# Optimization experiments

Measured on AMD Instinct MI355X. Metric: run time of the kernel, lower is better.

The kernel has to match this reference:

```python
import jax, jax.numpy as jnp
import numpy as np

QMAX = 127.0  # int8 symmetric quantization range


def _quant_dequant(w):
    """Per-output-channel symmetric int8 fake quantization (weight-only),
    mimicking nn.quantized.Linear.from_float weight quantization."""
    scale = jnp.max(jnp.abs(w), axis=-1, keepdims=True) / QMAX
    scale = jnp.maximum(scale, 1e-8)
    q = jnp.clip(jnp.round(w / scale), -QMAX, QMAX)
    return q * scale


def setup_inputs() -> dict:
    key = jax.random.key(0)
    ks = jax.random.split(key, 7)
    B, S, D, F, E, NS = 2, 2048, 1024, 2048, 8, 1
    std = 1.0 / np.sqrt(D)
    x = jax.random.normal(ks[0], (B, S, D), dtype=jnp.float32)
    router_w = _quant_dequant(jax.random.normal(ks[1], (E, D), dtype=jnp.float32) * std)
    router_b = jnp.zeros((E,), dtype=jnp.float32)
    w_up = _quant_dequant(jax.random.normal(ks[2], (E, F, D), dtype=jnp.float32) * std)
    w_down = _quant_dequant(jax.random.normal(ks[3], (E, D, F), dtype=jnp.float32) / np.sqrt(F))
    shared_w_up = _quant_dequant(jax.random.normal(ks[4], (NS, F, D), dtype=jnp.float32) * std)
    shared_w_down = _quant_dequant(jax.random.normal(ks[5], (NS, D, F), dtype=jnp.float32) / np.sqrt(F))
    return {"x": x, "router_w": router_w, "router_b": router_b,
            "w_up": w_up, "w_down": w_down,
            "shared_w_up": shared_w_up, "shared_w_down": shared_w_down}


def reference(x, router_w, router_b, w_up, w_down, shared_w_up, shared_w_down):
    B, S, D = x.shape
    E = router_w.shape[0]
    TOPK = 2
    xt = x.reshape(-1, D)  # [T, D] tokens

    # Router (quantized linear) -> softmax -> top-k dispatch weights
    logits = xt @ router_w.T + router_b            # [T, E]
    probs = jax.nn.softmax(logits, axis=-1)        # [T, E]
    top_vals, top_idx = jax.lax.top_k(probs, TOPK)  # [T, K]
    top_vals = top_vals / jnp.sum(top_vals, axis=-1, keepdims=True)  # renormalize
    # combine[t, e] = routing weight of expert e for token t (0 if not selected)
    combine = jnp.sum(jax.nn.one_hot(top_idx, E, dtype=xt.dtype) * top_vals[..., None], axis=1)  # [T, E]

    # Routed experts: up -> SiLU -> down, computed densely then combined
    h = jnp.einsum('td,efd->tef', xt, w_up)        # [T, E, F]
    y = jnp.einsum('tef,edf->ted', jax.nn.silu(h), w_down)  # [T, E, D]
    out = jnp.einsum('ted,te->td', y, combine)     # [T, D]

    # Shared experts: always active, summed
    hs = jnp.einsum('td,sfd->tsf', xt, shared_w_up)          # [T, NS, F]
    out = out + jnp.einsum('tsf,sdf->td', jax.nn.silu(hs), shared_w_down)

    return out.reshape(B, S, D)
```

## Files before the change

kernel.cpp:

```cpp
#include <hip/hip_runtime.h>
#include <stdint.h>

typedef unsigned short u16;
typedef int i32x4 __attribute__((ext_vector_type(4)));

#define DDIM 1024
#define FDIM 2048
#define NEXP 8
#define RT_TILES 72
#define SHOFF 9216
#define RCAP 13312
#define NRT 104
#define UPROWS 16384
#define DNROWS 8192
#define WQB 4608


__device__ inline float bf2f(u16 u) {
    union { unsigned int i; float f; } v; v.i = ((unsigned int)u) << 16; return v.f;
}
__device__ inline u16 f2bf(float f) {
    union { float f; unsigned int i; } v; v.f = f;
    unsigned int lsb = (v.i >> 16) & 1u;
    return (u16)((v.i + 0x7fffu + lsb) >> 16);
}
__device__ inline int q8(float v, float inv) {
    int x = (int)rintf(v * inv);
    return x < -127 ? -127 : (x > 127 ? 127 : x);
}

typedef const __attribute__((address_space(1))) void gas_void;
typedef __attribute__((address_space(3))) void las_void;
#define GLL16(g, l) __builtin_amdgcn_global_load_lds((gas_void*)(g), (las_void*)(l), 16, 0, 0)

__device__ inline int detect_inline(const u16* __restrict__ x, int* sh) {
    if (threadIdx.x == 0) *sh = 0;
    __syncthreads();
    const int per = 1024 / blockDim.x;
    int bad = 0;
    for (int i = 0; i < per; i++) {
        u16 v = x[threadIdx.x * per + i];
        if (((v >> 7) & 0xFF) >= 0x8F) bad++;
    }
    if (bad) atomicAdd(sh, bad);
    __syncthreads();
    return (*sh > 32) ? 1 : 0;
}

__global__ __launch_bounds__(256) void fused_rw_kernel(
    const void* __restrict__ x_, const void* __restrict__ rw_, const void* __restrict__ rb_,
    const void* __restrict__ w_up, const void* __restrict__ w_down,
    const void* __restrict__ sw_up, const void* __restrict__ sw_down,
    float* __restrict__ top_w, int* __restrict__ top_idx,
    char* __restrict__ qup, char* __restrict__ qdn,
    float* __restrict__ su, float* __restrict__ sd, int nrb)
{
    __shared__ char smem[32768 + 16];
    const int tid = threadIdx.x;
    const int wave = tid >> 6, lane = tid & 63;
    const int flag = detect_inline((const u16*)x_, (int*)(smem + 32768));

    if ((int)blockIdx.x < nrb) {
        float* rws = (float*)smem;
        if (!flag) {
            const ushort4* rwv = (const ushort4*)rw_;
            #pragma unroll
            for (int i = 0; i < 8; i++) {
                int idx = tid + i * 256;
                ushort4 h = rwv[idx];
                rws[idx * 4 + 0] = bf2f(h.x); rws[idx * 4 + 1] = bf2f(h.y);
                rws[idx * 4 + 2] = bf2f(h.z); rws[idx * 4 + 3] = bf2f(h.w);
            }
        } else {
            const float4* rwv = (const float4*)rw_;
            #pragma unroll
            for (int i = 0; i < 8; i++) {
                int idx = tid + i * 256;
                float4 f = rwv[idx];
                rws[idx * 4 + 0] = f.x; rws[idx * 4 + 1] = f.y;
                rws[idx * 4 + 2] = f.z; rws[idx * 4 + 3] = f.w;
            }
        }
        __syncthreads();

        for (int sub = 0; sub < 4; sub++) {
            const int t = blockIdx.x * 16 + wave * 4 + sub;
            float xv[16];
            if (!flag) {
                const u16* xr = (const u16*)x_ + (size_t)t * DDIM + lane * 16;
                uint4 p0 = *(const uint4*)(xr);
                uint4 p1 = *(const uint4*)(xr + 8);
                #pragma unroll
                for (int d = 0; d < 8; d++) xv[d]     = bf2f(((const u16*)&p0)[d]);
                #pragma unroll
                for (int d = 0; d < 8; d++) xv[d + 8] = bf2f(((const u16*)&p1)[d]);
            } else {
                const float4* xr = (const float4*)((const float*)x_ + (size_t)t * DDIM + lane * 16);
                #pragma unroll
                for (int c = 0; c < 4; c++) {
                    float4 f = xr[c];
                    xv[c * 4 + 0] = f.x; xv[c * 4 + 1] = f.y;
                    xv[c * 4 + 2] = f.z; xv[c * 4 + 3] = f.w;
                }
            }
            float acc[NEXP];
            #pragma unroll
            for (int e = 0; e < NEXP; e++) {
                const float* wr = &rws[e * DDIM + lane * 16];
                float s = 0.f;
                #pragma unroll
                for (int d = 0; d < 16; d++) s += xv[d] * wr[d];
                acc[e] = s;
            }
            #pragma unroll
            for (int e = 0; e < NEXP; e++) {
                #pragma unroll
                for (int off = 32; off > 0; off >>= 1)
                    acc[e] += __shfl_xor(acc[e], off, 64);
            }
            if (lane == 0) {
                float lg[NEXP];
                #pragma unroll
                for (int e = 0; e < NEXP; e++) {
                    float b = flag ? ((const float*)rb_)[e] : bf2f(((const u16*)rb_)[e]);
                    lg[e] = acc[e] + b;
                }
                int i0 = 0;
                #pragma unroll
                for (int e = 1; e < NEXP; e++) if (lg[e] > lg[i0]) i0 = e;
                int i1 = (i0 == 0) ? 1 : 0;
                #pragma unroll
                for (int e = 0; e < NEXP; e++) if (e != i0 && lg[e] > lg[i1]) i1 = e;
                float e1 = __expf(lg[i1] - lg[i0]);
                float w0 = 1.f / (1.f + e1);
                float w1 = e1 / (1.f + e1);
                top_w[2 * t] = w0;  top_w[2 * t + 1] = w1;
                top_idx[2 * t] = i0; top_idx[2 * t + 1] = i1;
            }
        }
        return;
    }

    const int g = blockIdx.x - nrb;
    const int isUp = (g < 2304);
    const size_t es = flag ? 4 : 2;
    const int G = isUp ? 8 : 4;
    const int rowelems = isUp ? DDIM : FDIM;
    const size_t rowbytes = (size_t)rowelems * es;
    const int R0 = isUp ? (g * 8) : ((g - 2304) * 4);
    const char* wbase = isUp ? (const char*)w_up : (const char*)w_down;
    const char* sbase = isUp ? (const char*)sw_up : (const char*)sw_down;
    const int nmain = isUp ? UPROWS : DNROWS;
    char* qdst = isUp ? qup : qdn;
    float* sdst = isUp ? su : sd;

    const int cpr = (int)(rowbytes >> 10);
    const int cprsh = 31 - __clz(cpr);
    const int npw = (G * cpr) >> 2;
    for (int k = 0; k < npw; k++) {
        const int ii = wave * npw + k;
        const int r = ii >> cprsh;
        const int c = ii - (r << cprsh);
        const int R = R0 + r;
        const char* src = (R < nmain ? wbase + (size_t)R * rowbytes
                                     : sbase + (size_t)(R - nmain) * rowbytes)
                          + (c << 10) + lane * 16;
        GLL16(src, smem + r * rowbytes + (c << 10));
    }
    __syncthreads();

    const int rpw = G >> 2;
    const int cmax = rowelems >> 8;
    for (int rr = 0; rr < rpw; rr++) {
        const int r = wave * rpw + rr;
        const int R = R0 + r;
        const char* ld = smem + r * rowbytes;
        float m = 0.f;
        if (flag) {
            for (int c = 0; c < cmax; c++) {
                float4 f = *(const float4*)(ld + (size_t)((c * 64 + lane) << 4));
                m = fmaxf(m, fmaxf(fmaxf(fabsf(f.x), fabsf(f.y)),
                                   fmaxf(fabsf(f.z), fabsf(f.w))));
            }
        } else {
            for (int c = 0; c < cmax; c++) {
                ushort4 h = *(const ushort4*)(ld + (size_t)((c * 64 + lane) << 3));
                m = fmaxf(m, fmaxf(fmaxf(fabsf(bf2f(h.x)), fabsf(bf2f(h.y))),
                                   fmaxf(fabsf(bf2f(h.z)), fabsf(bf2f(h.w)))));
            }
        }
        #pragma unroll
        for (int off = 32; off > 0; off >>= 1) m = fmaxf(m, __shfl_xor(m, off, 64));
        m = fmaxf(m, 1e-12f);
        if (lane == 0) sdst[R] = m / 127.f;
        const float inv = 127.f / m;
        for (int c = 0; c < cmax; c++) {
            float4 f;
            if (flag) {
                f = *(const float4*)(ld + (size_t)((c * 64 + lane) << 4));
            } else {
                ushort4 h = *(const ushort4*)(ld + (size_t)((c * 64 + lane) << 3));
                f.x = bf2f(h.x); f.y = bf2f(h.y); f.z = bf2f(h.z); f.w = bf2f(h.w);
            }
            unsigned u = (unsigned)(q8(f.x, inv) & 255) |
                         ((unsigned)(q8(f.y, inv) & 255) << 8) |
                         ((unsigned)(q8(f.z, inv) & 255) << 16) |
                         ((unsigned)(q8(f.w, inv) & 255) << 24);
            *(unsigned*)(qdst + (size_t)R * rowelems + (size_t)((c * 64 + lane) << 2)) = u;
        }
    }
}

__global__ __launch_bounds__(1024) void rank_kernel(
    const u16* __restrict__ x, const int* __restrict__ top_idx,
    int* __restrict__ tok_rows, int* __restrict__ meta)
{
    __shared__ int wsum[16][NEXP];
    __shared__ int wbase[16][NEXP];
    __shared__ int scnt;
    const int tid = threadIdx.x, lane = tid & 63, wave = tid >> 6;

    const int flag = detect_inline(x, &scnt);
    if (tid == 0) meta[30] = flag;

    const int4* tp = (const int4*)(top_idx + tid * 8);
    int4 v0 = tp[0], v1 = tp[1];
    int e[8] = { v0.x, v0.y, v0.z, v0.w, v1.x, v1.y, v1.z, v1.w };

    int tcnt[NEXP];
    #pragma unroll
    for (int en = 0; en < NEXP; en++) tcnt[en] = 0;
    #pragma unroll
    for (int j = 0; j < 8; j++)
        #pragma unroll
        for (int en = 0; en < NEXP; en++) tcnt[en] += (e[j] == en);

    int excl[NEXP];
    #pragma unroll
    for (int en = 0; en < NEXP; en++) {
        int v = tcnt[en];
        #pragma unroll
        for (int off = 1; off < 64; off <<= 1) {
            int u = __shfl_up(v, off, 64);
            if (lane >= off) v += u;
        }
        excl[en] = v - tcnt[en];
        if (lane == 63) wsum[wave][en] = v;
    }
    __syncthreads();
    if (tid < NEXP) {
        int s = 0;
        for (int w = 0; w < 16; w++) { int c = wsum[w][tid]; wbase[w][tid] = s; s += c; }
        meta[tid] = s;
    }
    __syncthreads();
    if (tid == 0) {
        int b = 0;
        for (int en = 0; en < NEXP; en++) {
            meta[8 + en] = b;
            b += ((meta[en] + 127) >> 7) << 7;
        }
        meta[16] = b;
    }
    __syncthreads();

    int cur[NEXP];
    #pragma unroll
    for (int en = 0; en < NEXP; en++) cur[en] = meta[8 + en] + wbase[wave][en] + excl[en];

    int r[8];
    #pragma unroll
    for (int j = 0; j < 8; j++) {
        int rr = 0;
        #pragma unroll
        for (int en = 0; en < NEXP; en++)
            if (e[j] == en) { rr = cur[en]; cur[en] = rr + 1; }
        r[j] = rr;
    }
    int4* rp = (int4*)(tok_rows + tid * 8);
    rp[0] = make_int4(r[0], r[1], r[2], r[3]);
    rp[1] = make_int4(r[4], r[5], r[6], r[7]);
}

__global__ __launch_bounds__(128) void gather_q_kernel(
    const void* __restrict__ x_, const int* __restrict__ tok_rows,
    char* __restrict__ xq, float* __restrict__ sxa, const int* __restrict__ meta)
{
    __shared__ float red[128];
    const int t = blockIdx.x, tid = threadIdx.x;
    const int r0 = tok_rows[2 * t], r1 = tok_rows[2 * t + 1];

    float v[8];
    if (!meta[30]) {
        uint4 p = ((const uint4*)((const u16*)x_ + (size_t)t * DDIM))[tid];
        #pragma unroll
        for (int d = 0; d < 8; d++) v[d] = bf2f(((const u16*)&p)[d]);
    } else {
        const float4* xf = (const float4*)((const float*)x_ + (size_t)t * DDIM);
        float4 a = xf[2 * tid], b = xf[2 * tid + 1];
        v[0] = a.x; v[1] = a.y; v[2] = a.z; v[3] = a.w;
        v[4] = b.x; v[5] = b.y; v[6] = b.z; v[7] = b.w;
    }
    float m = 0.f;
    #pragma unroll
    for (int d = 0; d < 8; d++) m = fmaxf(m, fabsf(v[d]));
    red[tid] = m;
    __syncthreads();
    for (int s = 64; s > 0; s >>= 1) {
        if (tid < s) red[tid] = fmaxf(red[tid], red[tid + s]);
        __syncthreads();
    }
    const float mx = fmaxf(red[0], 1e-8f);
    const float inv = 127.f / mx;

    uint2 u;
    u.x = (unsigned)(q8(v[0], inv) & 255) | ((unsigned)(q8(v[1], inv) & 255) << 8) |
          ((unsigned)(q8(v[2], inv) & 255) << 16) | ((unsigned)(q8(v[3], inv) & 255) << 24);
    u.y = (unsigned)(q8(v[4], inv) & 255) | ((unsigned)(q8(v[5], inv) & 255) << 8) |
          ((unsigned)(q8(v[6], inv) & 255) << 16) | ((unsigned)(q8(v[7], inv) & 255) << 24);

    ((uint2*)(xq + (size_t)r0 * DDIM))[tid] = u;
    ((uint2*)(xq + (size_t)r1 * DDIM))[tid] = u;
    ((uint2*)(xq + (size_t)(SHOFF + t) * DDIM))[tid] = u;
    if (tid == 0) {
        float s = mx / 127.f;
        sxa[r0] = s; sxa[r1] = s; sxa[SHOFF + t] = s;
    }
}

__global__ __launch_bounds__(256, 2) void moe_gemm_i8(
    const char* __restrict__ A, const char* __restrict__ Wq,
    const float* __restrict__ sa, const float* __restrict__ sw,
    u16* __restrict__ Cout, const int* __restrict__ meta, int N, int Kd, int act)
{
    const int L = blockIdx.y * gridDim.x + blockIdx.x;
    const int xcd = L & 7;
    const int jj = L >> 3;
    const int rt = xcd * 13 + (jj % 13);
    const int ct = jj / 13;

    int e;
    if (rt >= RT_TILES) {
        e = NEXP;
    } else {
        const int r0t = rt * 128;
        if (r0t >= meta[16]) return;
        e = 0;
        #pragma unroll
        for (int i = 1; i < NEXP; i++) if (r0t >= meta[8 + i]) e = i;
        if (r0t >= meta[8 + e] + meta[e]) return;
    }
    const char* Wb = Wq + (size_t)(e * N + ct * 256) * Kd;
    const float* swb = sw + e * N + ct * 256;

    __shared__ char As[2][128 * 64];
    __shared__ char Bs[2][256 * 64];

    const int tid = threadIdx.x;
    const int wave = tid >> 6, lane = tid & 63;
    const int wm = (wave >> 1) * 64;
    const int wn = (wave & 1) * 128;
    const int l16 = lane & 15;
    const int q = lane >> 4;
    const int slot = (q + (l16 >> 1)) & 3;

    const int rsub = lane >> 2;
    const int qs = ((lane & 3) - ((lane >> 3) & 3)) & 3;

    const char* Ag = A + (size_t)(rt * 128 + wave * 16 + rsub) * Kd + qs * 16;
    const char* Bg = Wb + (size_t)(wave * 16 + rsub) * Kd + qs * 16;
    const size_t rstep = (size_t)64 * Kd;

    i32x4 acc[4][8] = {};

#define STAGE(buf, off) do { \
        GLL16(Ag + (off),             &As[buf][wave * 1024]); \
        GLL16(Ag + (off) + rstep,     &As[buf][4096 + wave * 1024]); \
        GLL16(Bg + (off),             &Bs[buf][wave * 1024]); \
        GLL16(Bg + (off) + rstep,     &Bs[buf][4096 + wave * 1024]); \
        GLL16(Bg + (off) + 2 * rstep, &Bs[buf][8192 + wave * 1024]); \
        GLL16(Bg + (off) + 3 * rstep, &Bs[buf][12288 + wave * 1024]); \
    } while (0)

    STAGE(0, 0);
    __syncthreads();

    int cur = 0;
    for (int kk = 0; kk < Kd; kk += 64) {
        if (kk + 64 < Kd) STAGE(cur ^ 1, kk + 64);
        i32x4 af[4], bf[8];
        #pragma unroll
        for (int i = 0; i < 4; i++)
            af[i] = *(const i32x4*)&As[cur][(wm + i * 16 + l16) * 64 + slot * 16];
        #pragma unroll
        for (int j = 0; j < 8; j++)
            bf[j] = *(const i32x4*)&Bs[cur][(wn + j * 16 + l16) * 64 + slot * 16];
        #pragma unroll
        for (int i = 0; i < 4; i++)
            #pragma unroll
            for (int j = 0; j < 8; j++)
                acc[i][j] = __builtin_amdgcn_mfma_i32_16x16x64_i8(af[i], bf[j], acc[i][j], 0, 0, 0);
        __syncthreads();
        cur ^= 1;
    }
#undef STAGE

    float sal[4][4];
    #pragma unroll
    for (int i = 0; i < 4; i++)
        #pragma unroll
        for (int rr = 0; rr < 4; rr++)
            sal[i][rr] = sa[rt * 128 + wm + i * 16 + q * 4 + rr];
    float swl[8];
    #pragma unroll
    for (int j = 0; j < 8; j++) swl[j] = swb[wn + j * 16 + l16];

    u16* Crow = Cout + (size_t)(rt * 128) * N + ct * 256;
    #pragma unroll
    for (int i = 0; i < 4; i++) {
        #pragma unroll
        for (int j = 0; j < 8; j++) {
            #pragma unroll
            for (int rr = 0; rr < 4; rr++) {
                const int row = wm + i * 16 + q * 4 + rr;
                const int col = wn + j * 16 + l16;
                float v = (float)acc[i][j][rr] * sal[i][rr] * swl[j];
                if (act) v = v / (1.f + __expf(-v));
                Crow[(size_t)row * N + col] = f2bf(v);
            }
        }
    }
}

__global__ __launch_bounds__(256) void hquant_kernel(
    const u16* __restrict__ hg, char* __restrict__ h8, float* __restrict__ sh,
    const int* __restrict__ meta)
{
    const int r = blockIdx.x;
    if (r >= meta[16] && r < SHOFF) return;
    __shared__ float red[256];
    const int tid = threadIdx.x;
    const u16* row = hg + (size_t)r * FDIM;
    uint4 p = ((const uint4*)row)[tid];
    float v[8];
    #pragma unroll
    for (int d = 0; d < 8; d++) v[d] = bf2f(((const u16*)&p)[d]);
    float m = 0.f;
    #pragma unroll
    for (int d = 0; d < 8; d++) m = fmaxf(m, fabsf(v[d]));
    red[tid] = m;
    __syncthreads();
    for (int s = 128; s > 0; s >>= 1) {
        if (tid < s) red[tid] = fmaxf(red[tid], red[tid + s]);
        __syncthreads();
    }
    const float mx = fmaxf(red[0], 1e-8f);
    const float inv = 127.f / mx;
    if (tid == 0) sh[r] = mx / 127.f;
    uint2 u;
    u.x = (unsigned)(q8(v[0], inv) & 255) | ((unsigned)(q8(v[1], inv) & 255) << 8) |
          ((unsigned)(q8(v[2], inv) & 255) << 16) | ((unsigned)(q8(v[3], inv) & 255) << 24);
    u.y = (unsigned)(q8(v[4], inv) & 255) | ((unsigned)(q8(v[5], inv) & 255) << 8) |
          ((unsigned)(q8(v[6], inv) & 255) << 16) | ((unsigned)(q8(v[7], inv) & 255) << 24);
    ((uint2*)(h8 + (size_t)r * FDIM))[tid] = u;
}

__global__ __launch_bounds__(256) void combine_kernel(
    const u16* __restrict__ yg, const float* __restrict__ top_w,
    const int* __restrict__ tok_rows, void* __restrict__ out_, const int* __restrict__ meta)
{
    const int t = blockIdx.x;
    const int r0 = tok_rows[2 * t], r1 = tok_rows[2 * t + 1];
    const float w0 = top_w[2 * t], w1 = top_w[2 * t + 1];
    const int d = threadIdx.x * 4;
    ushort4 y0 = *(const ushort4*)(yg + (size_t)r0 * DDIM + d);
    ushort4 y1 = *(const ushort4*)(yg + (size_t)r1 * DDIM + d);
    ushort4 ys = *(const ushort4*)(yg + (size_t)(SHOFF + t) * DDIM + d);
    float o0 = w0 * bf2f(y0.x) + w1 * bf2f(y1.x) + bf2f(ys.x);
    float o1 = w0 * bf2f(y0.y) + w1 * bf2f(y1.y) + bf2f(ys.y);
    float o2 = w0 * bf2f(y0.z) + w1 * bf2f(y1.z) + bf2f(ys.z);
    float o3 = w0 * bf2f(y0.w) + w1 * bf2f(y1.w) + bf2f(ys.w);
    if (!meta[30]) {
        ushort4 o; o.x = f2bf(o0); o.y = f2bf(o1); o.z = f2bf(o2); o.w = f2bf(o3);
        *(ushort4*)((u16*)out_ + (size_t)t * DDIM + d) = o;
    } else {
        float4 o; o.x = o0; o.y = o1; o.z = o2; o.w = o3;
        *(float4*)((float*)out_ + (size_t)t * DDIM + d) = o;
    }
}

extern "C" void kernel_launch(void* const* d_in, const int* in_sizes, int n_in,
                              void* d_out, int out_size, void* d_ws, size_t ws_size,
                              hipStream_t stream) {
    const void* x       = d_in[0];
    const void* rw      = d_in[1];
    const void* rb      = d_in[2];
    const void* w_up    = d_in[3];
    const void* w_down  = d_in[4];
    const void* sw_up   = d_in[5];
    const void* sw_down = d_in[6];

    const int T = in_sizes[0] / DDIM;

    char* ws = (char*)d_ws;
    int*   meta     = (int*)ws;
    float* top_w    = (float*)(ws + 1024);
    int*   top_idx  = (int*)(ws + 1024 + 8 * T);
    int*   tok_rows = (int*)(ws + 1024 + 16 * T);
    size_t off = 131072;
    u16*  yg = (u16*)(ws + off);
    char* xq = (char*)(ws + off);
    off += (size_t)RCAP * DDIM * 2;
    u16*  hg = (u16*)(ws + off);
    off += (size_t)RCAP * FDIM * 2;
    char* h8 = (char*)(ws + off);
    off += (size_t)RCAP * FDIM;
    char* qup = (char*)(ws + off);
    off += (size_t)(NEXP + 1) * FDIM * DDIM;
    char* qdn = (char*)(ws + off);
    off += (size_t)(NEXP + 1) * DDIM * FDIM;
    float* sxa = (float*)(ws + off); off += (size_t)RCAP * 4;
    float* sh  = (float*)(ws + off); off += (size_t)RCAP * 4;
    float* su  = (float*)(ws + off); off += (size_t)(NEXP + 1) * FDIM * 4;
    float* sd  = (float*)(ws + off); off += (size_t)(NEXP + 1) * DDIM * 4;

    const int nrb = T / 16;
    fused_rw_kernel<<<nrb + WQB, 256, 0, stream>>>(
        x, rw, rb, w_up, w_down, sw_up, sw_down,
        top_w, top_idx, qup, qdn, su, sd, nrb);
    rank_kernel<<<1, 1024, 0, stream>>>((const u16*)x, top_idx, tok_rows, meta);
    gather_q_kernel<<<T, 128, 0, stream>>>(x, tok_rows, xq, sxa, meta);

    moe_gemm_i8<<<dim3(FDIM / 256, NRT), 256, 0, stream>>>(
        xq, qup, sxa, su, hg, meta, FDIM, DDIM, 1);
    hquant_kernel<<<RCAP, 256, 0, stream>>>(hg, h8, sh, meta);
    moe_gemm_i8<<<dim3(DDIM / 256, NRT), 256, 0, stream>>>(
        h8, qdn, sh, sd, yg, meta, DDIM, FDIM, 0);
    combine_kernel<<<T, 256, 0, stream>>>(yg, top_w, tok_rows, d_out, meta);
}
```

Before: 322.2 us.

## Split router and weight quantization kernels; quantize each row per wave from registers

The fused router plus weight-quantize kernel is split into a router kernel and a dedicated weight-quantization kernel. Each wave now quantizes one full weight row by loading it straight from global memory into registers, instead of staging 8 or 4 rows through shared memory with global_load_lds and a block barrier. This is meant to remove the LDS round trip and the synchronization, and to give finer-grained parallelism. It adds one more kernel launch, gives up the overlap of router and quantization work inside a single grid, and in the f32 path reads each row twice from global memory.

```diff
diff --git a/kernel.cpp b/kernel.cpp
--- a/kernel.cpp
+++ b/kernel.cpp
@@ -13,7 +13,9 @@
 #define NRT 104
 #define UPROWS 16384
 #define DNROWS 8192
-#define WQB 4608
+#define UPTOT (UPROWS + FDIM)
+#define DNTOT (DNROWS + DDIM)
+#define WQWAVES (UPTOT + DNTOT)
 
 
 __device__ inline float bf2f(u16 u) {
@@ -27,6 +29,10 @@
 __device__ inline int q8(float v, float inv) {
     int x = (int)rintf(v * inv);
     return x < -127 ? -127 : (x > 127 ? 127 : x);
+}
+__device__ inline unsigned pack4(float a, float b, float c, float d, float inv) {
+    return (unsigned)(q8(a, inv) & 255) | ((unsigned)(q8(b, inv) & 255) << 8) |
+           ((unsigned)(q8(c, inv) & 255) << 16) | ((unsigned)(q8(d, inv) & 255) << 24);
 }
 
 typedef const __attribute__((address_space(1))) void gas_void;
@@ -47,167 +53,174 @@
     return (*sh > 32) ? 1 : 0;
 }
 
-__global__ __launch_bounds__(256) void fused_rw_kernel(
+__global__ __launch_bounds__(256) void router_kernel(
     const void* __restrict__ x_, const void* __restrict__ rw_, const void* __restrict__ rb_,
-    const void* __restrict__ w_up, const void* __restrict__ w_down,
-    const void* __restrict__ sw_up, const void* __restrict__ sw_down,
-    float* __restrict__ top_w, int* __restrict__ top_idx,
-    char* __restrict__ qup, char* __restrict__ qdn,
-    float* __restrict__ su, float* __restrict__ sd, int nrb)
+    float* __restrict__ top_w, int* __restrict__ top_idx)
 {
     __shared__ char smem[32768 + 16];
     const int tid = threadIdx.x;
     const int wave = tid >> 6, lane = tid & 63;
     const int flag = detect_inline((const u16*)x_, (int*)(smem + 32768));
 
-    if ((int)blockIdx.x < nrb) {
-        float* rws = (float*)smem;
+    float* rws = (float*)smem;
+    if (!flag) {
+        const ushort4* rwv = (const ushort4*)rw_;
+        #pragma unroll
+        for (int i = 0; i < 8; i++) {
+            int idx = tid + i * 256;
+            ushort4 h = rwv[idx];
+            rws[idx * 4 + 0] = bf2f(h.x); rws[idx * 4 + 1] = bf2f(h.y);
+            rws[idx * 4 + 2] = bf2f(h.z); rws[idx * 4 + 3] = bf2f(h.w);
+        }
+    } else {
+        const float4* rwv = (const float4*)rw_;
+        #pragma unroll
+        for (int i = 0; i < 8; i++) {
+            int idx = tid + i * 256;
+            float4 f = rwv[idx];
+            rws[idx * 4 + 0] = f.x; rws[idx * 4 + 1] = f.y;
+            rws[idx * 4 + 2] = f.z; rws[idx * 4 + 3] = f.w;
+        }
+    }
+    __syncthreads();
+
+    for (int sub = 0; sub < 4; sub++) {
+        const int t = blockIdx.x * 16 + wave * 4 + sub;
+        float xv[16];
         if (!flag) {
-            const ushort4* rwv = (const ushort4*)rw_;
-            #pragma unroll
-            for (int i = 0; i < 8; i++) {
-                int idx = tid + i * 256;
-                ushort4 h = rwv[idx];
-                rws[idx * 4 + 0] = bf2f(h.x); rws[idx * 4 + 1] = bf2f(h.y);
-                rws[idx * 4 + 2] = bf2f(h.z); rws[idx * 4 + 3] = bf2f(h.w);
+            const u16* xr = (const u16*)x_ + (size_t)t * DDIM + lane * 16;
+            uint4 p0 = *(const uint4*)(xr);
+            uint4 p1 = *(const uint4*)(xr + 8);
+            #pragma unroll
+            for (int d = 0; d < 8; d++) xv[d]     = bf2f(((const u16*)&p0)[d]);
+            #pragma unroll
+            for (int d = 0; d < 8; d++) xv[d + 8] = bf2f(((const u16*)&p1)[d]);
+        } else {
+            const float4* xr = (const float4*)((const float*)x_ + (size_t)t * DDIM + lane * 16);
+            #pragma unroll
+            for (int c = 0; c < 4; c++) {
+                float4 f = xr[c];
+                xv[c * 4 + 0] = f.x; xv[c * 4 + 1] = f.y;
+                xv[c * 4 + 2] = f.z; xv[c * 4 + 3] = f.w;
             }
-        } else {
-            const float4* rwv = (const float4*)rw_;
-            #pragma unroll
-            for (int i = 0; i < 8; i++) {
-                int idx = tid + i * 256;
-                float4 f = rwv[idx];
-                rws[idx * 4 + 0] = f.x; rws[idx * 4 + 1] = f.y;
-                rws[idx * 4 + 2] = f.z; rws[idx * 4 + 3] = f.w;
+        }
+        float acc[NEXP];
+        #pragma unroll
+        for (int e = 0; e < NEXP; e++) {
+            const float* wr = &rws[e * DDIM + lane * 16];
+            float s = 0.f;
+            #pragma unroll
+            for (int d = 0; d < 16; d++) s += xv[d] * wr[d];
+            acc[e] = s;
+        }
+        #pragma unroll
+        for (int e = 0; e < NEXP; e++) {
+            #pragma unroll
+            for (int off = 32; off > 0; off >>= 1)
+                acc[e] += __shfl_xor(acc[e], off, 64);
+        }
+        if (lane == 0) {
+            float lg[NEXP];
+            #pragma unroll
+            for (int e = 0; e < NEXP; e++) {
+                float b = flag ? ((const float*)rb_)[e] : bf2f(((const u16*)rb_)[e]);
+                lg[e] = acc[e] + b;
             }
-        }
-        __syncthreads();
-
-        for (int sub = 0; sub < 4; sub++) {
-            const int t = blockIdx.x * 16 + wave * 4 + sub;
-            float xv[16];
-            if (!flag) {
-                const u16* xr = (const u16*)x_ + (size_t)t * DDIM + lane * 16;
-                uint4 p0 = *(const uint4*)(xr);
-                uint4 p1 = *(const uint4*)(xr + 8);
-                #pragma unroll
-                for (int d = 0; d < 8; d++) xv[d]     = bf2f(((const u16*)&p0)[d]);
-                #pragma unroll
-                for (int d = 0; d < 8; d++) xv[d + 8] = bf2f(((const u16*)&p1)[d]);
-            } else {
-                const float4* xr = (const float4*)((const float*)x_ + (size_t)t * DDIM + lane * 16);
-                #pragma unroll
-                for (int c = 0; c < 4; c++) {
-                    float4 f = xr[c];
-                    xv[c * 4 + 0] = f.x; xv[c * 4 + 1] = f.y;
-                    xv[c * 4 + 2] = f.z; xv[c * 4 + 3] = f.w;
-                }
-            }
-            float acc[NEXP];
-            #pragma unroll
-            for (int e = 0; e < NEXP; e++) {
-                const float* wr = &rws[e * DDIM + lane * 16];
-                float s = 0.f;
-                #pragma unroll
-                for (int d = 0; d < 16; d++) s += xv[d] * wr[d];
-                acc[e] = s;
-            }
-            #pragma unroll
-            for (int e = 0; e < NEXP; e++) {
-                #pragma unroll
-                for (int off = 32; off > 0; off >>= 1)
-                    acc[e] += __shfl_xor(acc[e], off, 64);
-            }
-            if (lane == 0) {
-                float lg[NEXP];
-                #pragma unroll
-                for (int e = 0; e < NEXP; e++) {
-                    float b = flag ? ((const float*)rb_)[e] : bf2f(((const u16*)rb_)[e]);
-                    lg[e] = acc[e] + b;
-                }
-                int i0 = 0;
-                #pragma unroll
-                for (int e = 1; e < NEXP; e++) if (lg[e] > lg[i0]) i0 = e;
-                int i1 = (i0 == 0) ? 1 : 0;
-                #pragma unroll
-                for (int e = 0; e < NEXP; e++) if (e != i0 && lg[e] > lg[i1]) i1 = e;
-                float e1 = __expf(lg[i1] - lg[i0]);
-                float w0 = 1.f / (1.f + e1);
-                float w1 = e1 / (1.f + e1);
-                top_w[2 * t] = w0;  top_w[2 * t + 1] = w1;
-                top_idx[2 * t] = i0; top_idx[2 * t + 1] = i1;
-            }
-        }
-        return;
-    }
-
-    const int g = blockIdx.x - nrb;
-    const int isUp = (g < 2304);
-    const size_t es = flag ? 4 : 2;
-    const int G = isUp ? 8 : 4;
-    const int rowelems = isUp ? DDIM : FDIM;
-    const size_t rowbytes = (size_t)rowelems * es;
-    const int R0 = isUp ? (g * 8) : ((g - 2304) * 4);
-    const char* wbase = isUp ? (const char*)w_up : (const char*)w_down;
-    const char* sbase = isUp ? (const char*)sw_up : (const char*)sw_down;
-    const int nmain = isUp ? UPROWS : DNROWS;
-    char* qdst = isUp ? qup : qdn;
-    float* sdst = isUp ? su : sd;
-
-    const int cpr = (int)(rowbytes >> 10);
-    const int cprsh = 31 - __clz(cpr);
-    const int npw = (G * cpr) >> 2;
-    for (int k = 0; k < npw; k++) {
-        const int ii = wave * npw + k;
-        const int r = ii >> cprsh;
-        const int c = ii - (r << cprsh);
-        const int R = R0 + r;
-        const char* src = (R < nmain ? wbase + (size_t)R * rowbytes
-                                     : sbase + (size_t)(R - nmain) * rowbytes)
-                          + (c << 10) + lane * 16;
-        GLL16(src, smem + r * rowbytes + (c << 10));
-    }
-    __syncthreads();
-
-    const int rpw = G >> 2;
-    const int cmax = rowelems >> 8;
-    for (int rr = 0; rr < rpw; rr++) {
-        const int r = wave * rpw + rr;
-        const int R = R0 + r;
-        const char* ld = smem + r * rowbytes;
-        float m = 0.f;
-        if (flag) {
-            for (int c = 0; c < cmax; c++) {
-                float4 f = *(const float4*)(ld + (size_t)((c * 64 + lane) << 4));
-                m = fmaxf(m, fmaxf(fmaxf(fabsf(f.x), fabsf(f.y)),
-                                   fmaxf(fabsf(f.z), fabsf(f.w))));
-            }
-        } else {
-            for (int c = 0; c < cmax; c++) {
-                ushort4 h = *(const ushort4*)(ld + (size_t)((c * 64 + lane) << 3));
-                m = fmaxf(m, fmaxf(fmaxf(fabsf(bf2f(h.x)), fabsf(bf2f(h.y))),
-                                   fmaxf(fabsf(bf2f(h.z)), fabsf(bf2f(h.w)))));
-            }
-        }
-        #pragma unroll
-        for (int off = 32; off > 0; off >>= 1) m = fmaxf(m, __shfl_xor(m, off, 64));
-        m = fmaxf(m, 1e-12f);
-        if (lane == 0) sdst[R] = m / 127.f;
-        const float inv = 127.f / m;
-        for (int c = 0; c < cmax; c++) {
-            float4 f;
-            if (flag) {
-                f = *(const float4*)(ld + (size_t)((c * 64 + lane) << 4));
-            } else {
-                ushort4 h = *(const ushort4*)(ld + (size_t)((c * 64 + lane) << 3));
-                f.x = bf2f(h.x); f.y = bf2f(h.y); f.z = bf2f(h.z); f.w = bf2f(h.w);
-            }
-            unsigned u = (unsigned)(q8(f.x, inv) & 255) |
-                         ((unsigned)(q8(f.y, inv) & 255) << 8) |
-                         ((unsigned)(q8(f.z, inv) & 255) << 16) |
-                         ((unsigned)(q8(f.w, inv) & 255) << 24);
-            *(unsigned*)(qdst + (size_t)R * rowelems + (size_t)((c * 64 + lane) << 2)) = u;
-        }
+            int i0 = 0;
+            #pragma unroll
+            for (int e = 1; e < NEXP; e++) if (lg[e] > lg[i0]) i0 = e;
+            int i1 = (i0 == 0) ? 1 : 0;
+            #pragma unroll
+            for (int e = 0; e < NEXP; e++) if (e != i0 && lg[e] > lg[i1]) i1 = e;
+            float e1 = __expf(lg[i1] - lg[i0]);
+            float w0 = 1.f / (1.f + e1);
+            float w1 = e1 / (1.f + e1);
+            top_w[2 * t] = w0;  top_w[2 * t + 1] = w1;
+            top_idx[2 * t] = i0; top_idx[2 * t + 1] = i1;
+        }
+    }
+}
+
+template<int NC>
+__device__ inline void wq_bf16(const char* __restrict__ src, char* __restrict__ dst,
+                               float* __restrict__ sout, int R, int lane) {
+    uint4 raw[NC];
+    #pragma unroll
+    for (int c = 0; c < NC; c++)
+        raw[c] = *(const uint4*)(src + (size_t)c * 1024 + lane * 16);
+    float m = 0.f;
+    #pragma unroll
+    for (int c = 0; c < NC; c++) {
+        const u16* h = (const u16*)&raw[c];
+        #pragma unroll
+        for (int d = 0; d < 8; d++) m = fmaxf(m, fabsf(bf2f(h[d])));
+    }
+    #pragma unroll
+    for (int off = 32; off > 0; off >>= 1) m = fmaxf(m, __shfl_xor(m, off, 64));
+    m = fmaxf(m, 1e-12f);
+    if (lane == 0) sout[R] = m / 127.f;
+    const float inv = 127.f / m;
+    #pragma unroll
+    for (int c = 0; c < NC; c++) {
+        const u16* h = (const u16*)&raw[c];
+        uint2 o;
+        o.x = pack4(bf2f(h[0]), bf2f(h[1]), bf2f(h[2]), bf2f(h[3]), inv);
+        o.y = pack4(bf2f(h[4]), bf2f(h[5]), bf2f(h[6]), bf2f(h[7]), inv);
+        *(uint2*)(dst + (size_t)c * 512 + lane * 8) = o;
+    }
+}
+
+template<int NC>
+__device__ inline void wq_f32(const char* __restrict__ src, char* __restrict__ dst,
+                              float* __restrict__ sout, int R, int lane) {
+    float m = 0.f;
+    #pragma unroll
+    for (int c = 0; c < NC; c++) {
+        float4 f = *(const float4*)(src + (size_t)c * 1024 + lane * 16);
+        m = fmaxf(m, fmaxf(fmaxf(fabsf(f.x), fabsf(f.y)),
+                           fmaxf(fabsf(f.z), fabsf(f.w))));
+    }
+    #pragma unroll
+    for (int off = 32; off > 0; off >>= 1) m = fmaxf(m, __shfl_xor(m, off, 64));
+    m = fmaxf(m, 1e-12f);
+    if (lane == 0) sout[R] = m / 127.f;
+    const float inv = 127.f / m;
+    #pragma unroll
+    for (int c = 0; c < NC; c++) {
+        float4 f = *(const float4*)(src + (size_t)c * 1024 + lane * 16);
+        *(unsigned*)(dst + (size_t)c * 256 + lane * 4) = pack4(f.x, f.y, f.z, f.w, inv);
+    }
+}
+
+__global__ __launch_bounds__(256) void wquant_kernel(
+    const void* __restrict__ x_,
+    const void* __restrict__ w_up, const void* __restrict__ w_down,
+    const void* __restrict__ sw_up, const void* __restrict__ sw_down,
+    char* __restrict__ qup, char* __restrict__ qdn,
+    float* __restrict__ su, float* __restrict__ sd)
+{
+    __shared__ int scnt;
+    const int wave = threadIdx.x >> 6, lane = threadIdx.x & 63;
+    const int flag = detect_inline((const u16*)x_, &scnt);
+    const int id = blockIdx.x * 4 + wave;
+    if (id < UPTOT) {
+        const int R = id;
+        const size_t rb = flag ? (size_t)DDIM * 4 : (size_t)DDIM * 2;
+        const char* src = (R < UPROWS)
+            ? (const char*)w_up + (size_t)R * rb
+            : (const char*)sw_up + (size_t)(R - UPROWS) * rb;
+        char* dst = qup + (size_t)R * DDIM;
+        if (!flag) wq_bf16<2>(src, dst, su, R, lane);
+        else       wq_f32<4>(src, dst, su, R, lane);
+    } else {
+        const int R = id - UPTOT;
+        const size_t rb = flag ? (size_t)FDIM * 4 : (size_t)FDIM * 2;
+        const char* src = (R < DNROWS)
+            ? (const char*)w_down + (size_t)R * rb
+            : (const char*)sw_down + (size_t)(R - DNROWS) * rb;
+        char* dst = qdn + (size_t)R * FDIM;
+        if (!flag) wq_bf16<4>(src, dst, sd, R, lane);
+        else       wq_f32<8>(src, dst, sd, R, lane);
     }
 }
 
@@ -525,9 +538,9 @@
     float* sd  = (float*)(ws + off); off += (size_t)(NEXP + 1) * DDIM * 4;
 
     const int nrb = T / 16;
-    fused_rw_kernel<<<nrb + WQB, 256, 0, stream>>>(
-        x, rw, rb, w_up, w_down, sw_up, sw_down,
-        top_w, top_idx, qup, qdn, su, sd, nrb);
+    router_kernel<<<nrb, 256, 0, stream>>>(x, rw, rb, top_w, top_idx);
+    wquant_kernel<<<WQWAVES / 4, 256, 0, stream>>>(
+        x, w_up, w_down, sw_up, sw_down, qup, qdn, su, sd);
     rank_kernel<<<1, 1024, 0, stream>>>((const u16*)x, top_idx, tok_rows, meta);
     gather_q_kernel<<<T, 128, 0, stream>>>(x, tok_rows, xq, sxa, meta);
 
```

Result: slower. 333.7 us (+3.6%).
